# Kernel optimization log

Measured on AMD Instinct MI355X. Metric: run time of the kernel, lower is better.

## Reference

```python
import jax, jax.numpy as jnp
import numpy as np

LN_EPS = 1e-5
L2_EPS = 1e-12  # torch F.normalize eps


def _layernorm(h, g, b):
    mu = jnp.mean(h, axis=-1, keepdims=True)
    var = jnp.var(h, axis=-1, keepdims=True)
    return (h - mu) * jax.lax.rsqrt(var + LN_EPS) * g + b


def _l2norm(h):
    n = jnp.linalg.norm(h, axis=-1, keepdims=True)
    return h / jnp.maximum(n, L2_EPS)


def _temperature(epoch, total_epochs):
    warmup = total_epochs * 0.1
    if epoch < warmup:
        return 2.0
    progress = (epoch - warmup) / (total_epochs - warmup)
    return max(0.7, 2.0 - 1.3 * progress)


def setup_inputs() -> dict:
    key = jax.random.key(0)
    ks = jax.random.split(key, 4)
    B, T, D, P, C = 8, 4096, 1024, 512, 64
    x = jax.random.normal(ks[0], (B, T, D), dtype=jnp.float32)
    w1 = jax.random.normal(ks[1], (D, C), dtype=jnp.float32) * 0.02
    b1 = jnp.zeros((C,), jnp.float32)
    ln1_g = jnp.ones((C,), jnp.float32)
    ln1_b = jnp.zeros((C,), jnp.float32)
    patterns = jax.random.normal(ks[2], (P, C), dtype=jnp.float32)
    patterns = _l2norm(patterns)  # init is row-orthonormalized in torch via SVD; unit rows suffice
    w2 = jax.random.normal(ks[3], (C, D), dtype=jnp.float32) * 0.02
    b2 = jnp.zeros((D,), jnp.float32)
    ln2_g = jnp.ones((D,), jnp.float32)
    ln2_b = jnp.zeros((D,), jnp.float32)
    return {"x": x, "w1": w1, "b1": b1, "ln1_g": ln1_g, "ln1_b": ln1_b,
            "patterns": patterns, "w2": w2, "b2": b2, "ln2_g": ln2_g, "ln2_b": ln2_b,
            "epoch": 0, "total_epochs": 100}


def reference(x, w1, b1, ln1_g, ln1_b, patterns, w2, b2, ln2_g, ln2_b, epoch, total_epochs):
    n_patterns = patterns.shape[0]
    # bottleneck projection + LayerNorm: [B,T,D] -> [B,T,C]
    Q = _layernorm(jnp.einsum('btd,dc->btc', x, w1) + b1, ln1_g, ln1_b)
    Q_norm = _l2norm(Q)
    K_norm = _l2norm(patterns)  # [P,C]
    temp = _temperature(epoch, total_epochs)
    logits = jnp.einsum('btc,pc->btp', Q_norm, K_norm) / temp  # [B,T,P]
    hard_indices = jnp.argmax(logits, axis=-1)  # [B,T]
    assignments = jax.nn.one_hot(hard_indices, n_patterns, dtype=jnp.float32)  # eval: hard
    pattern_emb_low = jnp.einsum('btp,pc->btc', assignments, patterns)
    pattern_emb = _layernorm(jnp.einsum('btc,cd->btd', pattern_emb_low, w2) + b2, ln2_g, ln2_b)
    return (pattern_emb, assignments, logits, hard_indices, Q)
```

## Files before the change

### kernel.cpp

```cpp
#include <hip/hip_runtime.h>

#define O_PE 0
#define O_AS 33554432
#define O_LG 50331648
#define O_HI 67108864
#define O_Q  67141632

__global__ void k0_pre(const float* __restrict__ patterns, const float* __restrict__ w2,
                       const float* __restrict__ b2, const float* __restrict__ ln2g,
                       const float* __restrict__ ln2b, const int* __restrict__ epoch,
                       const int* __restrict__ total_epochs,
                       float* __restrict__ invt, float* __restrict__ knT,
                       float* __restrict__ peb) {
  const int b = blockIdx.x, t = threadIdx.x;
  __shared__ float pat[64];
  __shared__ float red[8];

  if (b == 0 && t == 0) {
    float ep = (float)epoch[0], te = (float)total_epochs[0];
    float warm = te * 0.1f;
    float temp;
    if (ep < warm) temp = 2.0f;
    else {
      float prog = (ep - warm) / (te - warm);
      temp = fmaxf(0.7f, 2.0f - 1.3f * prog);
    }
    invt[0] = 1.0f / temp;
  }

  if (t < 64) pat[t] = patterns[b * 64 + t];
  __syncthreads();

  if (t < 64) {
    float v = pat[t];
    float s = v * v;
    #pragma unroll
    for (int m = 1; m < 64; m <<= 1) s += __shfl_xor(s, m);
    float scale = 1.0f / fmaxf(sqrtf(s), 1e-12f);
    knT[(size_t)t * 512 + b] = v * scale;
  }

  const int d0 = t * 4;
  float4 acc = *(const float4*)&b2[d0];
  #pragma unroll 8
  for (int k = 0; k < 64; ++k) {
    float pk = pat[k];
    float4 w = *(const float4*)&w2[(size_t)k * 1024 + d0];
    acc.x = fmaf(pk, w.x, acc.x);
    acc.y = fmaf(pk, w.y, acc.y);
    acc.z = fmaf(pk, w.z, acc.z);
    acc.w = fmaf(pk, w.w, acc.w);
  }
  float s1 = acc.x + acc.y + acc.z + acc.w;
  float s2 = acc.x*acc.x + acc.y*acc.y + acc.z*acc.z + acc.w*acc.w;
  #pragma unroll
  for (int m = 1; m < 64; m <<= 1) { s1 += __shfl_xor(s1, m); s2 += __shfl_xor(s2, m); }
  const int wid = t >> 6;
  if ((t & 63) == 0) { red[wid] = s1; red[wid + 4] = s2; }
  __syncthreads();
  s1 = red[0] + red[1] + red[2] + red[3];
  s2 = red[4] + red[5] + red[6] + red[7];
  float mu = s1 * (1.0f / 1024.0f);
  float var = s2 * (1.0f / 1024.0f) - mu * mu;
  float rstd = rsqrtf(var + 1e-5f);
  float4 g  = *(const float4*)&ln2g[d0];
  float4 bb = *(const float4*)&ln2b[d0];
  float4 o;
  o.x = (acc.x - mu) * rstd * g.x + bb.x;
  o.y = (acc.y - mu) * rstd * g.y + bb.y;
  o.z = (acc.z - mu) * rstd * g.z + bb.z;
  o.w = (acc.w - mu) * rstd * g.w + bb.w;
  *(float4*)&peb[(size_t)b * 1024 + d0] = o;
}

__global__ __launch_bounds__(256, 2) void k_fused(
    const float* __restrict__ x, const float* __restrict__ w1,
    const float* __restrict__ b1, const float* __restrict__ ln1g,
    const float* __restrict__ ln1b, const float* __restrict__ knT,
    const float* __restrict__ invtp, const float* __restrict__ peb,
    float* __restrict__ outPe, float* __restrict__ outAs,
    float* __restrict__ outLg, float* __restrict__ outHi,
    float* __restrict__ outQ) {
  __shared__ float smem[8704];
  const int tid = threadIdx.x;
  const int rowbase = blockIdx.x * 64;

  const int g  = tid >> 6;
  const int t  = tid & 63;
  const int rt = t >> 3, ct = t & 7;
  const int r0 = rt * 8, c0 = ct * 8;
  const int kbase = g * 256;

  float* xsT = smem;
  float* w1s = smem + 4352;

  float acc[8][8];
  #pragma unroll
  for (int i = 0; i < 8; ++i)
    #pragma unroll
    for (int j = 0; j < 8; ++j) acc[i][j] = 0.f;

  const int srow = t >> 2;
  const int skc4 = (t & 3) * 4;
  const int ssw  = 8 * ((skc4 >> 3) & 1);
  const float* xp = x + (size_t)(rowbase + srow) * 1024 + kbase + skc4;
  const int wkr = t >> 4;
  const int wc4 = (t & 15) * 4;
  const float* wp0 = w1 + (size_t)(kbase + wkr) * 64 + wc4;

  for (int kt = 0; kt < 16; ++kt) {
    const int kb = kt * 16;
    float4 xv[4], wv[4];
    #pragma unroll
    for (int p = 0; p < 4; ++p)
      xv[p] = *(const float4*)(xp + (size_t)p * 16384 + kb);
    #pragma unroll
    for (int p = 0; p < 4; ++p)
      wv[p] = *(const float4*)(wp0 + (size_t)(kb + 4 * p) * 64);
    __syncthreads();
    #pragma unroll
    for (int p = 0; p < 4; ++p) {
      const int row = (srow + 16 * p) ^ ssw;
      xsT[g*1088 + (skc4+0)*68 + row] = xv[p].x;
      xsT[g*1088 + (skc4+1)*68 + row] = xv[p].y;
      xsT[g*1088 + (skc4+2)*68 + row] = xv[p].z;
      xsT[g*1088 + (skc4+3)*68 + row] = xv[p].w;
    }
    #pragma unroll
    for (int p = 0; p < 4; ++p)
      *(float4*)&w1s[g*1088 + (wkr + 4*p)*68 + wc4] = wv[p];
    __syncthreads();
    #pragma unroll 4
    for (int kk = 0; kk < 16; ++kk) {
      const int rb = r0 ^ (8 * ((kk >> 3) & 1));
      float4 a0 = *(float4*)&xsT[g*1088 + kk*68 + rb];
      float4 a1 = *(float4*)&xsT[g*1088 + kk*68 + rb + 4];
      float4 b0 = *(float4*)&w1s[g*1088 + kk*68 + c0];
      float4 b1v = *(float4*)&w1s[g*1088 + kk*68 + c0 + 4];
      float av[8] = {a0.x, a0.y, a0.z, a0.w, a1.x, a1.y, a1.z, a1.w};
      float bv[8] = {b0.x, b0.y, b0.z, b0.w, b1v.x, b1v.y, b1v.z, b1v.w};
      #pragma unroll
      for (int i = 0; i < 8; ++i)
        #pragma unroll
        for (int j = 0; j < 8; ++j)
          acc[i][j] = fmaf(av[i], bv[j], acc[i][j]);
    }
  }

  float* qns  = smem;
  float* hacc = smem + 4352;
  float bb[8], gg[8], ee[8];
  if (g == 0) {
    float4 t0 = *(const float4*)&b1[c0];
    float4 t1 = *(const float4*)&b1[c0 + 4];
    float4 t2 = *(const float4*)&ln1g[c0];
    float4 t3 = *(const float4*)&ln1g[c0 + 4];
    float4 t4 = *(const float4*)&ln1b[c0];
    float4 t5 = *(const float4*)&ln1b[c0 + 4];
    bb[0]=t0.x; bb[1]=t0.y; bb[2]=t0.z; bb[3]=t0.w; bb[4]=t1.x; bb[5]=t1.y; bb[6]=t1.z; bb[7]=t1.w;
    gg[0]=t2.x; gg[1]=t2.y; gg[2]=t2.z; gg[3]=t2.w; gg[4]=t3.x; gg[5]=t3.y; gg[6]=t3.z; gg[7]=t3.w;
    ee[0]=t4.x; ee[1]=t4.y; ee[2]=t4.z; ee[3]=t4.w; ee[4]=t5.x; ee[5]=t5.y; ee[6]=t5.z; ee[7]=t5.w;
  }
  #pragma unroll
  for (int p2 = 0; p2 < 4; ++p2) {
    __syncthreads();
    if (g > 0 && (rt >> 1) == p2) {
      float* hc = hacc + (g - 1) * 1024 + (r0 - 16 * p2) * 64 + c0;
      #pragma unroll
      for (int i = 0; i < 8; ++i) {
        float4 v0, v1;
        v0.x = acc[i][0]; v0.y = acc[i][1]; v0.z = acc[i][2]; v0.w = acc[i][3];
        v1.x = acc[i][4]; v1.y = acc[i][5]; v1.z = acc[i][6]; v1.w = acc[i][7];
        *(float4*)(hc + i * 64)     = v0;
        *(float4*)(hc + i * 64 + 4) = v1;
      }
    }
    __syncthreads();
    if (g == 0 && (rt >> 1) == p2) {
      #pragma unroll
      for (int i = 0; i < 8; ++i) {
        const int row = r0 + i;
        float h[8];
        #pragma unroll
        for (int j = 0; j < 8; ++j) h[j] = acc[i][j] + bb[j];
        #pragma unroll
        for (int gg2 = 0; gg2 < 3; ++gg2) {
          float4 p0 = *(float4*)&hacc[gg2*1024 + (row - 16*p2)*64 + c0];
          float4 p1 = *(float4*)&hacc[gg2*1024 + (row - 16*p2)*64 + c0 + 4];
          h[0] += p0.x; h[1] += p0.y; h[2] += p0.z; h[3] += p0.w;
          h[4] += p1.x; h[5] += p1.y; h[6] += p1.z; h[7] += p1.w;
        }
        float s1 = 0.f, s2 = 0.f;
        #pragma unroll
        for (int j = 0; j < 8; ++j) { s1 += h[j]; s2 += h[j]*h[j]; }
        #pragma unroll
        for (int m = 1; m < 8; m <<= 1) { s1 += __shfl_xor(s1, m); s2 += __shfl_xor(s2, m); }
        const float mu   = s1 * 0.015625f;
        const float var  = s2 * 0.015625f - mu * mu;
        const float rstd = rsqrtf(var + 1e-5f);
        float q[8]; float t2s = 0.f;
        #pragma unroll
        for (int j = 0; j < 8; ++j) { q[j] = (h[j] - mu) * rstd * gg[j] + ee[j]; t2s += q[j]*q[j]; }
        #pragma unroll
        for (int m = 1; m < 8; m <<= 1) t2s += __shfl_xor(t2s, m);
        const float scl = 1.0f / fmaxf(sqrtf(t2s), 1e-12f);
        float4 qa, qc;
        qa.x = q[0]; qa.y = q[1]; qa.z = q[2]; qa.w = q[3];
        qc.x = q[4]; qc.y = q[5]; qc.z = q[6]; qc.w = q[7];
        *(float4*)&outQ[(size_t)(rowbase + row) * 64 + c0]     = qa;
        *(float4*)&outQ[(size_t)(rowbase + row) * 64 + c0 + 4] = qc;
        #pragma unroll
        for (int j = 0; j < 8; ++j) qns[row*68 + c0 + j] = q[j] * scl;
      }
    }
  }
  __syncthreads();

  const float invt = invtp[0];
  const int lane = tid & 63;
  const int w    = tid >> 6;
  const int brt  = lane & 3;
  const int pt16 = lane >> 2;
  const int pbase = w * 128 + pt16 * 8;

  float* avm = smem + 4352;
  int*   avi = (int*)(smem + 4608);
  int*   sidx = (int*)(smem + 4864);

  float a2[16][8];
  #pragma unroll
  for (int i = 0; i < 16; ++i)
    #pragma unroll
    for (int j = 0; j < 8; ++j) a2[i][j] = 0.f;

  for (int cb = 0; cb < 16; ++cb) {
    float kv[4][8];
    #pragma unroll
    for (int dc = 0; dc < 4; ++dc) {
      float4 k0 = *(const float4*)&knT[(size_t)(cb*4+dc)*512 + pbase];
      float4 k1 = *(const float4*)&knT[(size_t)(cb*4+dc)*512 + pbase + 4];
      kv[dc][0]=k0.x; kv[dc][1]=k0.y; kv[dc][2]=k0.z; kv[dc][3]=k0.w;
      kv[dc][4]=k1.x; kv[dc][5]=k1.y; kv[dc][6]=k1.z; kv[dc][7]=k1.w;
    }
    #pragma unroll
    for (int i = 0; i < 16; ++i) {
      float4 qv = *(float4*)&qns[(brt + 4*i)*68 + cb*4];
      float qq[4] = {qv.x, qv.y, qv.z, qv.w};
      #pragma unroll
      for (int dc = 0; dc < 4; ++dc)
        #pragma unroll
        for (int j = 0; j < 8; ++j)
          a2[i][j] = fmaf(qq[dc], kv[dc][j], a2[i][j]);
    }
  }

  #pragma unroll
  for (int i = 0; i < 16; ++i) {
    const int row = brt + 4*i;
    const size_t grow = (size_t)(rowbase + row);
    float v[8];
    float bm = -3.0e38f; int bi = 0;
    #pragma unroll
    for (int j = 0; j < 8; ++j) {
      v[j] = a2[i][j] * invt;
      if (v[j] > bm) { bm = v[j]; bi = pbase + j; }
    }
    float4 o0, o1;
    o0.x = v[0]; o0.y = v[1]; o0.z = v[2]; o0.w = v[3];
    o1.x = v[4]; o1.y = v[5]; o1.z = v[6]; o1.w = v[7];
    *(float4*)&outLg[grow * 512 + pbase]     = o0;
    *(float4*)&outLg[grow * 512 + pbase + 4] = o1;
    #pragma unroll
    for (int m = 4; m < 64; m <<= 1) {
      float ov = __shfl_xor(bm, m);
      int   oi = __shfl_xor(bi, m);
      if (ov > bm || (ov == bm && oi < bi)) { bm = ov; bi = oi; }
    }
    if (pt16 == 0) { avm[w*64 + row] = bm; avi[w*64 + row] = bi; }
  }
  __syncthreads();

  if (tid < 64) {
    float bm = avm[tid]; int bi = avi[tid];
    #pragma unroll
    for (int w2 = 1; w2 < 4; ++w2) {
      float m = avm[w2*64 + tid];
      int   i = avi[w2*64 + tid];
      if (m > bm) { bm = m; bi = i; }
    }
    sidx[tid] = bi;
    outHi[rowbase + tid] = (float)bi;
  }
  __syncthreads();

  #pragma unroll
  for (int p = 0; p < 32; ++p) {
    const int id = tid + p * 256;
    const int r = id >> 7, c4 = (id & 127) * 4;
    const int b = sidx[r];
    float4 z; z.x = 0.f; z.y = 0.f; z.z = 0.f; z.w = 0.f;
    if (b >= c4 && b < c4 + 4) ((float*)&z)[b - c4] = 1.0f;
    *(float4*)&outAs[(size_t)(rowbase + r) * 512 + c4] = z;
  }

  const float4* peb4 = (const float4*)peb;
  float4* o4 = (float4*)outPe;
  #pragma unroll 4
  for (int p = 0; p < 64; ++p) {
    const int id = tid + p * 256;
    const int r = id >> 8, c4 = id & 255;
    o4[(size_t)(rowbase + r) * 256 + c4] = peb4[(size_t)sidx[r] * 256 + c4];
  }
}

extern "C" void kernel_launch(void* const* d_in, const int* in_sizes, int n_in,
                              void* d_out, int out_size, void* d_ws, size_t ws_size,
                              hipStream_t stream) {
  (void)in_sizes; (void)n_in; (void)out_size; (void)ws_size;
  const float* x        = (const float*)d_in[0];
  const float* w1       = (const float*)d_in[1];
  const float* b1       = (const float*)d_in[2];
  const float* ln1g     = (const float*)d_in[3];
  const float* ln1b     = (const float*)d_in[4];
  const float* patterns = (const float*)d_in[5];
  const float* w2       = (const float*)d_in[6];
  const float* b2       = (const float*)d_in[7];
  const float* ln2g     = (const float*)d_in[8];
  const float* ln2b     = (const float*)d_in[9];
  const int*   epoch    = (const int*)d_in[10];
  const int*   total    = (const int*)d_in[11];

  float* out = (float*)d_out;
  float* outPe = out + O_PE;
  float* outAs = out + O_AS;
  float* outLg = out + O_LG;
  float* outHi = out + O_HI;
  float* outQ  = out + O_Q;

  float* wsf  = (float*)d_ws;
  float* invt = wsf;
  float* knT  = wsf + 64;
  float* peb  = (float*)((char*)d_ws + 131328);

  hipLaunchKernelGGL(k0_pre, dim3(512), dim3(256), 0, stream,
                     patterns, w2, b2, ln2g, ln2b, epoch, total, invt, knT, peb);
  hipLaunchKernelGGL(k_fused, dim3(512), dim3(256), 0, stream,
                     x, w1, b1, ln1g, ln1b, knT, invt, peb,
                     outPe, outAs, outLg, outHi, outQ);
}
```

Measured before the change: 170.8 us.

## Halve rows per block and split-K eight ways to double grid size

Each block of the fused kernel now handles 32 rows instead of 64, and the K dimension of the first GEMM is split across 8 groups of 128 instead of 4 groups of 256. The grid grows to 1024 blocks, which gives better occupancy and balance across the GPU's compute units. Shared memory drops and the per-thread logits tile halves. The cost is a larger cross-group reduction (7 partials instead of 3) and more blocks re-reading w1.

```diff
diff --git a/kernel.cpp b/kernel.cpp
--- a/kernel.cpp
+++ b/kernel.cpp
@@ -81,18 +81,18 @@
     float* __restrict__ outPe, float* __restrict__ outAs,
     float* __restrict__ outLg, float* __restrict__ outHi,
     float* __restrict__ outQ) {
-  __shared__ float smem[8704];
+  __shared__ float smem[6656];
   const int tid = threadIdx.x;
-  const int rowbase = blockIdx.x * 64;
-
-  const int g  = tid >> 6;
-  const int t  = tid & 63;
+  const int rowbase = blockIdx.x * 32;
+
+  const int g  = tid >> 5;
+  const int t  = tid & 31;
   const int rt = t >> 3, ct = t & 7;
   const int r0 = rt * 8, c0 = ct * 8;
-  const int kbase = g * 256;
+  const int kbase = g * 128;
 
   float* xsT = smem;
-  float* w1s = smem + 4352;
+  float* w1s = smem + 2304;
 
   float acc[8][8];
   #pragma unroll
@@ -100,43 +100,38 @@
     #pragma unroll
     for (int j = 0; j < 8; ++j) acc[i][j] = 0.f;
 
-  const int srow = t >> 2;
-  const int skc4 = (t & 3) * 4;
-  const int ssw  = 8 * ((skc4 >> 3) & 1);
-  const float* xp = x + (size_t)(rowbase + srow) * 1024 + kbase + skc4;
-  const int wkr = t >> 4;
-  const int wc4 = (t & 15) * 4;
-  const float* wp0 = w1 + (size_t)(kbase + wkr) * 64 + wc4;
+  const float* xp = x + (size_t)(rowbase + t) * 1024 + kbase;
+  const int wkr = t >> 3;
+  const int wc  = (t & 7) * 8;
+  const float* wp = w1 + (size_t)(kbase + wkr) * 64 + wc;
 
   for (int kt = 0; kt < 16; ++kt) {
-    const int kb = kt * 16;
-    float4 xv[4], wv[4];
-    #pragma unroll
-    for (int p = 0; p < 4; ++p)
-      xv[p] = *(const float4*)(xp + (size_t)p * 16384 + kb);
-    #pragma unroll
-    for (int p = 0; p < 4; ++p)
-      wv[p] = *(const float4*)(wp0 + (size_t)(kb + 4 * p) * 64);
+    float4 xv0 = *(const float4*)(xp + kt * 8);
+    float4 xv1 = *(const float4*)(xp + kt * 8 + 4);
+    float4 wv00 = *(const float4*)(wp + (size_t)kt * 512);
+    float4 wv01 = *(const float4*)(wp + (size_t)kt * 512 + 4);
+    float4 wv10 = *(const float4*)(wp + (size_t)kt * 512 + 256);
+    float4 wv11 = *(const float4*)(wp + (size_t)kt * 512 + 260);
     __syncthreads();
-    #pragma unroll
-    for (int p = 0; p < 4; ++p) {
-      const int row = (srow + 16 * p) ^ ssw;
-      xsT[g*1088 + (skc4+0)*68 + row] = xv[p].x;
-      xsT[g*1088 + (skc4+1)*68 + row] = xv[p].y;
-      xsT[g*1088 + (skc4+2)*68 + row] = xv[p].z;
-      xsT[g*1088 + (skc4+3)*68 + row] = xv[p].w;
-    }
-    #pragma unroll
-    for (int p = 0; p < 4; ++p)
-      *(float4*)&w1s[g*1088 + (wkr + 4*p)*68 + wc4] = wv[p];
+    xsT[g*288 + 0*36 + t] = xv0.x;
+    xsT[g*288 + 1*36 + t] = xv0.y;
+    xsT[g*288 + 2*36 + t] = xv0.z;
+    xsT[g*288 + 3*36 + t] = xv0.w;
+    xsT[g*288 + 4*36 + t] = xv1.x;
+    xsT[g*288 + 5*36 + t] = xv1.y;
+    xsT[g*288 + 6*36 + t] = xv1.z;
+    xsT[g*288 + 7*36 + t] = xv1.w;
+    *(float4*)&w1s[g*544 + wkr*68 + wc]         = wv00;
+    *(float4*)&w1s[g*544 + wkr*68 + wc + 4]     = wv01;
+    *(float4*)&w1s[g*544 + (wkr+4)*68 + wc]     = wv10;
+    *(float4*)&w1s[g*544 + (wkr+4)*68 + wc + 4] = wv11;
     __syncthreads();
-    #pragma unroll 4
-    for (int kk = 0; kk < 16; ++kk) {
-      const int rb = r0 ^ (8 * ((kk >> 3) & 1));
-      float4 a0 = *(float4*)&xsT[g*1088 + kk*68 + rb];
-      float4 a1 = *(float4*)&xsT[g*1088 + kk*68 + rb + 4];
-      float4 b0 = *(float4*)&w1s[g*1088 + kk*68 + c0];
-      float4 b1v = *(float4*)&w1s[g*1088 + kk*68 + c0 + 4];
+    #pragma unroll
+    for (int kk = 0; kk < 8; ++kk) {
+      float4 a0 = *(float4*)&xsT[g*288 + kk*36 + r0];
+      float4 a1 = *(float4*)&xsT[g*288 + kk*36 + r0 + 4];
+      float4 b0 = *(float4*)&w1s[g*544 + kk*68 + c0];
+      float4 b1v = *(float4*)&w1s[g*544 + kk*68 + c0 + 4];
       float av[8] = {a0.x, a0.y, a0.z, a0.w, a1.x, a1.y, a1.z, a1.w};
       float bv[8] = {b0.x, b0.y, b0.z, b0.w, b1v.x, b1v.y, b1v.z, b1v.w};
       #pragma unroll
@@ -148,7 +143,7 @@
   }
 
   float* qns  = smem;
-  float* hacc = smem + 4352;
+  float* hacc = smem + 2304;
   float bb[8], gg[8], ee[8];
   if (g == 0) {
     float4 t0 = *(const float4*)&b1[c0];
@@ -164,8 +159,8 @@
   #pragma unroll
   for (int p2 = 0; p2 < 4; ++p2) {
     __syncthreads();
-    if (g > 0 && (rt >> 1) == p2) {
-      float* hc = hacc + (g - 1) * 1024 + (r0 - 16 * p2) * 64 + c0;
+    if (g > 0 && rt == p2) {
+      float* hc = hacc + (g - 1) * 512 + c0;
       #pragma unroll
       for (int i = 0; i < 8; ++i) {
         float4 v0, v1;
@@ -176,7 +171,7 @@
       }
     }
     __syncthreads();
-    if (g == 0 && (rt >> 1) == p2) {
+    if (g == 0 && rt == p2) {
       #pragma unroll
       for (int i = 0; i < 8; ++i) {
         const int row = r0 + i;
@@ -184,9 +179,9 @@
         #pragma unroll
         for (int j = 0; j < 8; ++j) h[j] = acc[i][j] + bb[j];
         #pragma unroll
-        for (int gg2 = 0; gg2 < 3; ++gg2) {
-          float4 p0 = *(float4*)&hacc[gg2*1024 + (row - 16*p2)*64 + c0];
-          float4 p1 = *(float4*)&hacc[gg2*1024 + (row - 16*p2)*64 + c0 + 4];
+        for (int g2 = 0; g2 < 7; ++g2) {
+          float4 p0 = *(float4*)&hacc[g2*512 + i*64 + c0];
+          float4 p1 = *(float4*)&hacc[g2*512 + i*64 + c0 + 4];
           h[0] += p0.x; h[1] += p0.y; h[2] += p0.z; h[3] += p0.w;
           h[4] += p1.x; h[5] += p1.y; h[6] += p1.z; h[7] += p1.w;
         }
@@ -223,13 +218,13 @@
   const int pt16 = lane >> 2;
   const int pbase = w * 128 + pt16 * 8;
 
-  float* avm = smem + 4352;
-  int*   avi = (int*)(smem + 4608);
-  int*   sidx = (int*)(smem + 4864);
-
-  float a2[16][8];
-  #pragma unroll
-  for (int i = 0; i < 16; ++i)
+  float* avm = smem + 2304;
+  int*   avi = (int*)(smem + 2432);
+  int*   sidx = (int*)(smem + 2560);
+
+  float a2[8][8];
+  #pragma unroll
+  for (int i = 0; i < 8; ++i)
     #pragma unroll
     for (int j = 0; j < 8; ++j) a2[i][j] = 0.f;
 
@@ -243,7 +238,7 @@
       kv[dc][4]=k1.x; kv[dc][5]=k1.y; kv[dc][6]=k1.z; kv[dc][7]=k1.w;
     }
     #pragma unroll
-    for (int i = 0; i < 16; ++i) {
+    for (int i = 0; i < 8; ++i) {
       float4 qv = *(float4*)&qns[(brt + 4*i)*68 + cb*4];
       float qq[4] = {qv.x, qv.y, qv.z, qv.w};
       #pragma unroll
@@ -255,7 +250,7 @@
   }
 
   #pragma unroll
-  for (int i = 0; i < 16; ++i) {
+  for (int i = 0; i < 8; ++i) {
     const int row = brt + 4*i;
     const size_t grow = (size_t)(rowbase + row);
     float v[8];
@@ -276,16 +271,16 @@
       int   oi = __shfl_xor(bi, m);
       if (ov > bm || (ov == bm && oi < bi)) { bm = ov; bi = oi; }
     }
-    if (pt16 == 0) { avm[w*64 + row] = bm; avi[w*64 + row] = bi; }
-  }
-  __syncthreads();
-
-  if (tid < 64) {
+    if (pt16 == 0) { avm[w*32 + row] = bm; avi[w*32 + row] = bi; }
+  }
+  __syncthreads();
+
+  if (tid < 32) {
     float bm = avm[tid]; int bi = avi[tid];
     #pragma unroll
     for (int w2 = 1; w2 < 4; ++w2) {
-      float m = avm[w2*64 + tid];
-      int   i = avi[w2*64 + tid];
+      float m = avm[w2*32 + tid];
+      int   i = avi[w2*32 + tid];
       if (m > bm) { bm = m; bi = i; }
     }
     sidx[tid] = bi;
@@ -294,7 +289,7 @@
   __syncthreads();
 
   #pragma unroll
-  for (int p = 0; p < 32; ++p) {
+  for (int p = 0; p < 16; ++p) {
     const int id = tid + p * 256;
     const int r = id >> 7, c4 = (id & 127) * 4;
     const int b = sidx[r];
@@ -306,7 +301,7 @@
   const float4* peb4 = (const float4*)peb;
   float4* o4 = (float4*)outPe;
   #pragma unroll 4
-  for (int p = 0; p < 64; ++p) {
+  for (int p = 0; p < 32; ++p) {
     const int id = tid + p * 256;
     const int r = id >> 8, c4 = id & 255;
     o4[(size_t)(rowbase + r) * 256 + c4] = peb4[(size_t)sidx[r] * 256 + c4];
@@ -344,7 +339,7 @@
 
   hipLaunchKernelGGL(k0_pre, dim3(512), dim3(256), 0, stream,
                      patterns, w2, b2, ln2g, ln2b, epoch, total, invt, knT, peb);
-  hipLaunchKernelGGL(k_fused, dim3(512), dim3(256), 0, stream,
+  hipLaunchKernelGGL(k_fused, dim3(1024), dim3(256), 0, stream,
                      x, w1, b1, ln1g, ln1b, knT, invt, peb,
                      outPe, outAs, outLg, outHi, outQ);
 }
```

Result: slower. 187.3 us (+9.6%).
